# Performance work log

Hardware: AMD Instinct MI355X
Metric: run time of the kernel (lower is better)

## Reference

```python
import jax, jax.numpy as jnp
import numpy as np

N_NODES = 100000
N_EDGES = 1600000
IN_CH = 48
OUT_CH = 64
K = 2


def setup_inputs() -> dict:
    key = jax.random.key(0)
    k1, k2, k3, k4 = jax.random.split(key, 4)
    x = jax.random.normal(k1, (N_NODES, IN_CH), dtype=jnp.float32)
    edge_index = jax.random.randint(k2, (2, N_EDGES), 0, N_NODES, dtype=jnp.int64)
    W = jax.random.normal(k3, (IN_CH, OUT_CH), dtype=jnp.float32) * (1.0 / np.sqrt(IN_CH))
    b = jax.random.normal(k4, (OUT_CH,), dtype=jnp.float32) * 0.01
    return {"x": x, "edge_index": edge_index, "W": W, "b": b}


def _propagate(x, row, col):
    n = x.shape[0]
    # degree of each node counted over col (destination) indices
    deg = jax.ops.segment_sum(jnp.ones_like(col, dtype=x.dtype), col, num_segments=n)
    deg_inv_sqrt = jnp.where(deg > 0, jax.lax.rsqrt(jnp.where(deg > 0, deg, 1.0)), 0.0)
    norm = deg_inv_sqrt[row] * deg_inv_sqrt[col]  # [E]
    # gather-scale-scatter: out[col] += x[row] * norm
    msgs = x[row] * norm[:, None]  # [E, d]
    return jax.ops.segment_sum(msgs, col, num_segments=n)


def reference(x, edge_index, W, b):
    row, col = edge_index[0], edge_index[1]
    h = x
    for _ in range(K):
        h = _propagate(h, row, col)
    return h @ W + b
```

## Files before the change

### kernel.cpp

```cpp
#include <hip/hip_runtime.h>
#include <hip/hip_bf16.h>
#include <hip/hip_fp16.h>


#define N_NODES 100000
#define N_EDGES 1600000
#define IN_CH 48
#define OUT_CH 64
#define NBUCKETS 392
#define CAP 4608
#define EPB 8192
#define NBLK_EDGE 196
#define NBLK_BKT 391

__global__ void init_kernel(int* __restrict__ bucketCursor, int* __restrict__ binTotal) {
    int t = threadIdx.x;
    if (t < NBUCKETS) bucketCursor[t] = t * CAP;
    if (t < 64) binTotal[t] = 0;
}

__global__ void bucket_scatter_kernel(const int* __restrict__ row, const int* __restrict__ col,
                                      int* __restrict__ bucketCursor, int* __restrict__ edge_packed) {
    __shared__ int lh[NBUCKETS];
    __shared__ int lofs[NBUCKETS];
    __shared__ int lbase[NBUCKETS];
    __shared__ int stage[EPB];
    __shared__ unsigned short sbkt[EPB];
    __shared__ int wsum[4];
    int tid = threadIdx.x;
    int base = blockIdx.x * EPB;
    for (int i = tid; i < NBUCKETS; i += 256) lh[i] = 0;
    __syncthreads();
    #pragma unroll 4
    for (int k = 0; k < 32; k++) {
        int e = base + k * 256 + tid;
        if (e < N_EDGES) atomicAdd(&lh[col[e] >> 8], 1);
    }
    __syncthreads();
    {
        int c0 = (tid < 196) ? lh[2 * tid] : 0;
        int c1 = (tid < 196) ? lh[2 * tid + 1] : 0;
        int s = c0 + c1;
        int incl = s;
        int lane = tid & 63, w = tid >> 6;
        #pragma unroll
        for (int o = 1; o < 64; o <<= 1) {
            int v = __shfl_up(incl, o, 64);
            if (lane >= o) incl += v;
        }
        if (lane == 63) wsum[w] = incl;
        __syncthreads();
        int wbase = 0;
        for (int k = 0; k < w; k++) wbase += wsum[k];
        int ex = wbase + incl - s;
        if (tid < 196) {
            lofs[2 * tid]     = ex;
            lofs[2 * tid + 1] = ex + c0;
        }
    }
    __syncthreads();
    for (int i = tid; i < NBUCKETS; i += 256) {
        int c = lh[i];
        if (c > 0) lbase[i] = atomicAdd(&bucketCursor[i], c);
        lh[i] = 0;
    }
    __syncthreads();
    #pragma unroll 4
    for (int k = 0; k < 32; k++) {
        int e = base + k * 256 + tid;
        if (e < N_EDGES) {
            int c = col[e];
            int bkt = c >> 8;
            int r = atomicAdd(&lh[bkt], 1);
            int slot = lofs[bkt] + r;
            stage[slot] = (row[e] << 8) | (c & 255);
            sbkt[slot] = (unsigned short)bkt;
        }
    }
    __syncthreads();
    int total = (base + EPB <= N_EDGES) ? EPB : (N_EDGES - base);
    for (int i = tid; i < total; i += 256) {
        int bkt = sbkt[i];
        int dst = lbase[bkt] + (i - lofs[bkt]);
        if (dst < (bkt + 1) * CAP)
            edge_packed[dst] = stage[i];
    }
}

__global__ void fine_sort_kernel(const int* __restrict__ edge_packed,
                                 const int* __restrict__ bucketCursor,
                                 const float* __restrict__ x,
                                 int* __restrict__ edge_src,
                                 int* __restrict__ deg, int* __restrict__ start,
                                 float* __restrict__ dis, int* __restrict__ binTotal,
                                 __half2* __restrict__ xs) {
    __shared__ int fh[256];
    __shared__ int sfh[257];
    __shared__ int cur[256];
    __shared__ int bh[64];
    __shared__ float fdis[256];
    int b = blockIdx.x;
    int t = threadIdx.x;
    int s0 = b * CAP;
    int s1 = min(bucketCursor[b], (b + 1) * CAP);
    int nodeBase = b << 8;
    fh[t] = 0;
    if (t < 64) bh[t] = 0;
    __syncthreads();
    for (int j = s0 + t; j < s1; j += 256)
        atomicAdd(&fh[edge_packed[j] & 255], 1);
    __syncthreads();
    if (t == 0) {
        int s = 0;
        for (int k = 0; k < 256; k++) { sfh[k] = s; s += fh[k]; }
        sfh[256] = s;
    }
    __syncthreads();
    int node = nodeBase + t;
    bool valid = (node < N_NODES);
    int d = fh[t];
    float dv = (valid && d > 0) ? rsqrtf((float)d) : 0.0f;
    cur[t] = sfh[t];
    fdis[t] = dv;
    if (valid) {
        deg[node] = d;
        start[node] = s0 + sfh[t];
        dis[node] = dv;
        atomicAdd(&bh[min(d, 63)], 1);
    }
    __syncthreads();
    for (int i = t; i < 256 * 24; i += 256) {
        int ln = i / 24;
        int nd = nodeBase + ln;
        if (nd < N_NODES) {
            int ci = i - ln * 24;
            float dd = fdis[ln];
            float2 v = ((const float2*)x)[nd * 24 + ci];
            xs[nd * 24 + ci] = __floats2half2_rn(v.x * dd, v.y * dd);
        }
    }
    for (int j = s0 + t; j < s1; j += 256) {
        int rc = edge_packed[j];
        int p = atomicAdd(&cur[rc & 255], 1);
        edge_src[s0 + p] = rc >> 8;
    }
    __syncthreads();
    if (t < 64 && bh[t]) atomicAdd(&binTotal[t], bh[t]);
}

__global__ void binscan_kernel(const int* __restrict__ binTotal, int* __restrict__ binCursor) {
    if (threadIdx.x == 0) {
        int s = 0;
        for (int k = 63; k >= 0; k--) { binCursor[k] = s; s += binTotal[k]; }
    }
}

__global__ void order_kernel(const int* __restrict__ deg, const int* __restrict__ start,
                             const float* __restrict__ dis, int* __restrict__ binCursor,
                             int4* __restrict__ nodeinfo, int n) {
    __shared__ int lhist[64];
    __shared__ int lbase[64];
    int i = blockIdx.x * 256 + threadIdx.x;
    if (threadIdx.x < 64) lhist[threadIdx.x] = 0;
    __syncthreads();
    int bin = 0, myrank = 0;
    if (i < n) {
        bin = min(deg[i], 63);
        myrank = atomicAdd(&lhist[bin], 1);
    }
    __syncthreads();
    if (threadIdx.x < 64 && lhist[threadIdx.x] > 0)
        lbase[threadIdx.x] = atomicAdd(&binCursor[threadIdx.x], lhist[threadIdx.x]);
    __syncthreads();
    if (i < n)
        nodeinfo[lbase[bin] + myrank] = make_int4(i, start[i], deg[i], __float_as_int(dis[i]));
}

#define LOAD3(p, v0, v1, v2) { v0 = (p)[0]; v1 = (p)[1]; v2 = (p)[2]; }
#define ACC6(v0, v1, v2) { \
    float2 u0 = __half22float2(v0), u1 = __half22float2(v1), u2 = __half22float2(v2); \
    a0 += u0.x; a1 += u0.y; a2 += u1.x; a3 += u1.y; a4 += u2.x; a5 += u2.y; }
#define ACC6B(v0, v1, v2) { \
    float2 u0 = __half22float2(v0), u1 = __half22float2(v1), u2 = __half22float2(v2); \
    b0 += u0.x; b1 += u0.y; b2 += u1.x; b3 += u1.y; b4 += u2.x; b5 += u2.y; }

__global__ void gather1_kernel(const __half2* __restrict__ xs,
                               const int* __restrict__ edge_src,
                               const int4* __restrict__ nodeinfo,
                               __half2* __restrict__ h1) {
    int g = blockIdx.x * 32 + (threadIdx.x >> 3);
    int lane = threadIdx.x & 7;
    int4 ni = nodeinfo[g];
    int node = ni.x, s = ni.y, e = s + ni.z;
    float dv = __int_as_float(ni.w);
    float a0 = 0, a1 = 0, a2 = 0, a3 = 0, a4 = 0, a5 = 0;
    float b0 = 0, b1 = 0, b2 = 0, b3 = 0, b4 = 0, b5 = 0;
    int j = s;
    for (; j + 3 < e; j += 4) {
        int s0 = edge_src[j], s1 = edge_src[j + 1], s2 = edge_src[j + 2], s3 = edge_src[j + 3];
        const __half2* p0 = xs + s0 * 24 + lane * 3;
        const __half2* p1 = xs + s1 * 24 + lane * 3;
        const __half2* p2 = xs + s2 * 24 + lane * 3;
        const __half2* p3 = xs + s3 * 24 + lane * 3;
        __half2 v00,v01,v02, v10,v11,v12, v20,v21,v22, v30,v31,v32;
        LOAD3(p0, v00, v01, v02); LOAD3(p1, v10, v11, v12);
        LOAD3(p2, v20, v21, v22); LOAD3(p3, v30, v31, v32);
        ACC6(v00, v01, v02); ACC6B(v10, v11, v12);
        ACC6(v20, v21, v22); ACC6B(v30, v31, v32);
    }
    for (; j < e; ++j) {
        const __half2* p0 = xs + edge_src[j] * 24 + lane * 3;
        __half2 v00, v01, v02;
        LOAD3(p0, v00, v01, v02);
        ACC6(v00, v01, v02);
    }
    a0 += b0; a1 += b1; a2 += b2; a3 += b3; a4 += b4; a5 += b5;
    float sc = dv * dv;
    __half2* q = h1 + node * 24 + lane * 3;
    q[0] = __floats2half2_rn(a0 * sc, a1 * sc);
    q[1] = __floats2half2_rn(a2 * sc, a3 * sc);
    q[2] = __floats2half2_rn(a4 * sc, a5 * sc);
}

__global__ void gather2_gemm_kernel(const __half2* __restrict__ h1,
                                    const int* __restrict__ edge_src,
                                    const int4* __restrict__ nodeinfo,
                                    const float* __restrict__ W,
                                    const float* __restrict__ bias,
                                    float* __restrict__ out) {
    __shared__ float sW[IN_CH * OUT_CH];
    __shared__ float sb[OUT_CH];
    __shared__ float sh[32][IN_CH + 1];

    for (int i = threadIdx.x; i < IN_CH * OUT_CH; i += 256) sW[i] = W[i];
    if (threadIdx.x < OUT_CH) sb[threadIdx.x] = bias[threadIdx.x];

    int nl = threadIdx.x >> 3;
    int lane = threadIdx.x & 7;
    int g = blockIdx.x * 32 + nl;
    int4 ni = nodeinfo[g];
    int node = ni.x, s = ni.y, e = s + ni.z;
    float dv = __int_as_float(ni.w);

    float a0 = 0, a1 = 0, a2 = 0, a3 = 0, a4 = 0, a5 = 0;
    float b0 = 0, b1 = 0, b2 = 0, b3 = 0, b4 = 0, b5 = 0;
    int j = s;
    for (; j + 3 < e; j += 4) {
        int s0 = edge_src[j], s1 = edge_src[j + 1], s2 = edge_src[j + 2], s3 = edge_src[j + 3];
        const __half2* p0 = h1 + s0 * 24 + lane * 3;
        const __half2* p1 = h1 + s1 * 24 + lane * 3;
        const __half2* p2 = h1 + s2 * 24 + lane * 3;
        const __half2* p3 = h1 + s3 * 24 + lane * 3;
        __half2 v00,v01,v02, v10,v11,v12, v20,v21,v22, v30,v31,v32;
        LOAD3(p0, v00, v01, v02); LOAD3(p1, v10, v11, v12);
        LOAD3(p2, v20, v21, v22); LOAD3(p3, v30, v31, v32);
        ACC6(v00, v01, v02); ACC6B(v10, v11, v12);
        ACC6(v20, v21, v22); ACC6B(v30, v31, v32);
    }
    for (; j < e; ++j) {
        const __half2* p0 = h1 + edge_src[j] * 24 + lane * 3;
        __half2 v00, v01, v02;
        LOAD3(p0, v00, v01, v02);
        ACC6(v00, v01, v02);
    }
    a0 += b0; a1 += b1; a2 += b2; a3 += b3; a4 += b4; a5 += b5;
    int c0 = 6 * lane;
    sh[nl][c0 + 0] = a0 * dv;
    sh[nl][c0 + 1] = a1 * dv;
    sh[nl][c0 + 2] = a2 * dv;
    sh[nl][c0 + 3] = a3 * dv;
    sh[nl][c0 + 4] = a4 * dv;
    sh[nl][c0 + 5] = a5 * dv;
    __syncthreads();

    int j0 = lane * 8;
    float acc[8];
    #pragma unroll
    for (int i = 0; i < 8; i++) acc[i] = sb[j0 + i];
    for (int k = 0; k < IN_CH; k++) {
        float s0 = sh[nl][k];
        #pragma unroll
        for (int i = 0; i < 8; i++) acc[i] += s0 * sW[k * OUT_CH + j0 + i];
    }
    float4* o = (float4*)(out + (size_t)node * OUT_CH + j0);
    o[0] = make_float4(acc[0], acc[1], acc[2], acc[3]);
    o[1] = make_float4(acc[4], acc[5], acc[6], acc[7]);
}

extern "C" void kernel_launch(void* const* d_in, const int* in_sizes, int n_in,
                              void* d_out, int out_size, void* d_ws, size_t ws_size,
                              hipStream_t stream) {
    const float* x   = (const float*)d_in[0];
    const int*   ei  = (const int*)d_in[1];
    const float* W   = (const float*)d_in[2];
    const float* b   = (const float*)d_in[3];
    float* out = (float*)d_out;

    const int* row = ei;
    const int* col = ei + N_EDGES;

    int* ws_i = (int*)d_ws;
    int* bucketCursor = ws_i;
    int* binTotal     = ws_i + 512;
    int* binCursor    = ws_i + 576;
    int* deg          = ws_i + 1024;
    int* start        = ws_i + 101376;
    float* dis        = (float*)(ws_i + 201728);
    int4* nodeinfo    = (int4*)(ws_i + 302080);
    int* edge_packed  = ws_i + 703488;
    int* edge_src     = ws_i + 2509824;
    __half2* xs       = (__half2*)(ws_i + 4316160);
    __half2* h1       = (__half2*)(ws_i + 6716160);

    init_kernel<<<1, 512, 0, stream>>>(bucketCursor, binTotal);
    bucket_scatter_kernel<<<NBLK_EDGE, 256, 0, stream>>>(row, col, bucketCursor, edge_packed);
    fine_sort_kernel<<<NBLK_BKT, 256, 0, stream>>>(edge_packed, bucketCursor, x,
                                                   edge_src, deg, start, dis, binTotal, xs);
    binscan_kernel<<<1, 64, 0, stream>>>(binTotal, binCursor);
    order_kernel<<<(N_NODES + 255) / 256, 256, 0, stream>>>(deg, start, dis, binCursor,
                                                            nodeinfo, N_NODES);

    gather1_kernel<<<N_NODES / 32, 256, 0, stream>>>(xs, edge_src, nodeinfo, h1);
    gather2_gemm_kernel<<<N_NODES / 32, 256, 0, stream>>>(h1, edge_src, nodeinfo, W, b, out);
}
```

Before: 233.6 us.

## Software-pipeline neighbor gathers and parallelize fine-sort prefix scan

The gather loops in both propagation kernels now double-buffer groups of four neighbor rows, issuing the next group's loads before accumulating the current one, so more memory requests are in flight per thread. Separately, the serial single-thread prefix sum in the fine sort kernel becomes a wave-shuffle scan with a small cross-wave combine. The pipelining roughly doubles live registers per thread, which can lower occupancy.

```diff
diff --git a/kernel.cpp b/kernel.cpp
--- a/kernel.cpp
+++ b/kernel.cpp
@@ -95,10 +95,10 @@
                                  float* __restrict__ dis, int* __restrict__ binTotal,
                                  __half2* __restrict__ xs) {
     __shared__ int fh[256];
-    __shared__ int sfh[257];
     __shared__ int cur[256];
     __shared__ int bh[64];
     __shared__ float fdis[256];
+    __shared__ int wsum2[4];
     int b = blockIdx.x;
     int t = threadIdx.x;
     int s0 = b * CAP;
@@ -110,21 +110,31 @@
     for (int j = s0 + t; j < s1; j += 256)
         atomicAdd(&fh[edge_packed[j] & 255], 1);
     __syncthreads();
-    if (t == 0) {
-        int s = 0;
-        for (int k = 0; k < 256; k++) { sfh[k] = s; s += fh[k]; }
-        sfh[256] = s;
-    }
-    __syncthreads();
+    int c = fh[t];
+    int incl = c;
+    {
+        int sl = t & 63, sw = t >> 6;
+        #pragma unroll
+        for (int o = 1; o < 64; o <<= 1) {
+            int v = __shfl_up(incl, o, 64);
+            if (sl >= o) incl += v;
+        }
+        if (sl == 63) wsum2[sw] = incl;
+        __syncthreads();
+        int wbase = 0;
+        for (int k = 0; k < sw; k++) wbase += wsum2[k];
+        incl += wbase;
+    }
+    int ex = incl - c;
     int node = nodeBase + t;
     bool valid = (node < N_NODES);
-    int d = fh[t];
+    int d = c;
     float dv = (valid && d > 0) ? rsqrtf((float)d) : 0.0f;
-    cur[t] = sfh[t];
+    cur[t] = ex;
     fdis[t] = dv;
     if (valid) {
         deg[node] = d;
-        start[node] = s0 + sfh[t];
+        start[node] = s0 + ex;
         dis[node] = dv;
         atomicAdd(&bh[min(d, 63)], 1);
     }
@@ -184,39 +194,79 @@
     float2 u0 = __half22float2(v0), u1 = __half22float2(v1), u2 = __half22float2(v2); \
     b0 += u0.x; b1 += u0.y; b2 += u1.x; b3 += u1.y; b4 += u2.x; b5 += u2.y; }
 
+#define DECLD(P) __half2 P##00,P##01,P##02,P##10,P##11,P##12,P##20,P##21,P##22,P##30,P##31,P##32
+#define DECLS(S) int S##0, S##1, S##2, S##3
+#define LOADSRC(S) { S##0 = edge_src[j]; S##1 = edge_src[j+1]; \
+                     S##2 = edge_src[j+2]; S##3 = edge_src[j+3]; j += 4; }
+#define ISSUED(P, S, basep) { \
+    const __half2* q0 = basep + S##0 * 24 + lane3; \
+    const __half2* q1 = basep + S##1 * 24 + lane3; \
+    const __half2* q2 = basep + S##2 * 24 + lane3; \
+    const __half2* q3 = basep + S##3 * 24 + lane3; \
+    P##00 = q0[0]; P##01 = q0[1]; P##02 = q0[2]; \
+    P##10 = q1[0]; P##11 = q1[1]; P##12 = q1[2]; \
+    P##20 = q2[0]; P##21 = q2[1]; P##22 = q2[2]; \
+    P##30 = q3[0]; P##31 = q3[1]; P##32 = q3[2]; }
+#define CONSUMED(P) { ACC6(P##00,P##01,P##02); ACC6B(P##10,P##11,P##12); \
+                      ACC6(P##20,P##21,P##22); ACC6B(P##30,P##31,P##32); }
+
+#define GATHER_PIPELINE(basep) { \
+    int m = (e - s) >> 2; \
+    DECLD(A); DECLD(B); \
+    DECLS(sa); DECLS(sb); \
+    if (m >= 2) { \
+        LOADSRC(sa); LOADSRC(sb); \
+        ISSUED(A, sa, basep); \
+        m -= 2; \
+        while (m >= 2) { \
+            LOADSRC(sa); \
+            ISSUED(B, sb, basep); \
+            CONSUMED(A); \
+            LOADSRC(sb); \
+            ISSUED(A, sa, basep); \
+            CONSUMED(B); \
+            m -= 2; \
+        } \
+        if (m == 1) { \
+            LOADSRC(sa); \
+            ISSUED(B, sb, basep); \
+            CONSUMED(A); \
+            ISSUED(A, sa, basep); \
+            CONSUMED(B); \
+            CONSUMED(A); \
+        } else { \
+            ISSUED(B, sb, basep); \
+            CONSUMED(A); \
+            CONSUMED(B); \
+        } \
+    } else if (m == 1) { \
+        LOADSRC(sa); \
+        ISSUED(A, sa, basep); \
+        CONSUMED(A); \
+    } \
+    for (; j < e; ++j) { \
+        const __half2* p0 = basep + edge_src[j] * 24 + lane3; \
+        __half2 v00, v01, v02; \
+        LOAD3(p0, v00, v01, v02); \
+        ACC6(v00, v01, v02); \
+    } \
+    a0 += b0; a1 += b1; a2 += b2; a3 += b3; a4 += b4; a5 += b5; }
+
 __global__ void gather1_kernel(const __half2* __restrict__ xs,
                                const int* __restrict__ edge_src,
                                const int4* __restrict__ nodeinfo,
                                __half2* __restrict__ h1) {
     int g = blockIdx.x * 32 + (threadIdx.x >> 3);
-    int lane = threadIdx.x & 7;
+    int lane3 = (threadIdx.x & 7) * 3;
     int4 ni = nodeinfo[g];
     int node = ni.x, s = ni.y, e = s + ni.z;
     float dv = __int_as_float(ni.w);
     float a0 = 0, a1 = 0, a2 = 0, a3 = 0, a4 = 0, a5 = 0;
     float b0 = 0, b1 = 0, b2 = 0, b3 = 0, b4 = 0, b5 = 0;
     int j = s;
-    for (; j + 3 < e; j += 4) {
-        int s0 = edge_src[j], s1 = edge_src[j + 1], s2 = edge_src[j + 2], s3 = edge_src[j + 3];
-        const __half2* p0 = xs + s0 * 24 + lane * 3;
-        const __half2* p1 = xs + s1 * 24 + lane * 3;
-        const __half2* p2 = xs + s2 * 24 + lane * 3;
-        const __half2* p3 = xs + s3 * 24 + lane * 3;
-        __half2 v00,v01,v02, v10,v11,v12, v20,v21,v22, v30,v31,v32;
-        LOAD3(p0, v00, v01, v02); LOAD3(p1, v10, v11, v12);
-        LOAD3(p2, v20, v21, v22); LOAD3(p3, v30, v31, v32);
-        ACC6(v00, v01, v02); ACC6B(v10, v11, v12);
-        ACC6(v20, v21, v22); ACC6B(v30, v31, v32);
-    }
-    for (; j < e; ++j) {
-        const __half2* p0 = xs + edge_src[j] * 24 + lane * 3;
-        __half2 v00, v01, v02;
-        LOAD3(p0, v00, v01, v02);
-        ACC6(v00, v01, v02);
-    }
-    a0 += b0; a1 += b1; a2 += b2; a3 += b3; a4 += b4; a5 += b5;
+    GATHER_PIPELINE(xs);
     float sc = dv * dv;
-    __half2* q = h1 + node * 24 + lane * 3;
+    __half2* q = h1 + node * 24 + lane3;
     q[0] = __floats2half2_rn(a0 * sc, a1 * sc);
     q[1] = __floats2half2_rn(a2 * sc, a3 * sc);
     q[2] = __floats2half2_rn(a4 * sc, a5 * sc);
@@ -237,6 +287,7 @@
 
     int nl = threadIdx.x >> 3;
     int lane = threadIdx.x & 7;
+    int lane3 = lane * 3;
     int g = blockIdx.x * 32 + nl;
     int4 ni = nodeinfo[g];
     int node = ni.x, s = ni.y, e = s + ni.z;
@@ -245,25 +296,7 @@
     float a0 = 0, a1 = 0, a2 = 0, a3 = 0, a4 = 0, a5 = 0;
     float b0 = 0, b1 = 0, b2 = 0, b3 = 0, b4 = 0, b5 = 0;
     int j = s;
-    for (; j + 3 < e; j += 4) {
-        int s0 = edge_src[j], s1 = edge_src[j + 1], s2 = edge_src[j + 2], s3 = edge_src[j + 3];
-        const __half2* p0 = h1 + s0 * 24 + lane * 3;
-        const __half2* p1 = h1 + s1 * 24 + lane * 3;
-        const __half2* p2 = h1 + s2 * 24 + lane * 3;
-        const __half2* p3 = h1 + s3 * 24 + lane * 3;
-        __half2 v00,v01,v02, v10,v11,v12, v20,v21,v22, v30,v31,v32;
-        LOAD3(p0, v00, v01, v02); LOAD3(p1, v10, v11, v12);
-        LOAD3(p2, v20, v21, v22); LOAD3(p3, v30, v31, v32);
-        ACC6(v00, v01, v02); ACC6B(v10, v11, v12);
-        ACC6(v20, v21, v22); ACC6B(v30, v31, v32);
-    }
-    for (; j < e; ++j) {
-        const __half2* p0 = h1 + edge_src[j] * 24 + lane * 3;
-        __half2 v00, v01, v02;
-        LOAD3(p0, v00, v01, v02);
-        ACC6(v00, v01, v02);
-    }
-    a0 += b0; a1 += b1; a2 += b2; a3 += b3; a4 += b4; a5 += b5;
+    GATHER_PIPELINE(h1);
     int c0 = 6 * lane;
     sh[nl][c0 + 0] = a0 * dv;
     sh[nl][c0 + 1] = a1 * dv;
```

Measured after the change: 228.2 us. 1.02x faster.
